# Optimization experiments

Hardware: AMD Instinct MI355X
Metric: run time of the kernel (lower is better)

The kernel has to match this reference:

```python
import jax, jax.numpy as jnp
import numpy as np

V, E, D, T, B = 32000, 512, 512, 512, 32
PAD = 3

def layer_norm(x, g, b, eps=1e-5):
    m = jnp.mean(x, axis=-1, keepdims=True)
    v = jnp.mean((x - m) ** 2, axis=-1, keepdims=True)
    return (x - m) * jax.lax.rsqrt(v + eps) * g + b

def sru_direction(U, v, b, reverse):
    # U: (T, B, 4D) -> splits: x_tilde, f-gate pre-act, r-gate pre-act, highway input
    x_t, uf, ur, xp = jnp.split(U, 4, axis=-1)
    def step(c, inp):
        xt, uft, urt, xpt = inp
        f = jax.nn.sigmoid(uft + v[0] * c + b[0])
        r = jax.nn.sigmoid(urt + v[1] * c + b[1])
        c_new = f * c + (1.0 - f) * xt
        h = r * c_new + (1.0 - r) * xpt
        return c_new, h
    c0 = jnp.zeros((U.shape[1], v.shape[1]), U.dtype)  # (B, D)
    c_last, hs = jax.lax.scan(step, c0, (x_t, uf, ur, xp), reverse=reverse)
    return hs, c_last

def setup_inputs() -> dict:
    key = jax.random.key(0)
    ks = jax.random.split(key, 8)
    def rn(k, shp, sc=0.05):
        return jax.random.normal(k, shp, jnp.float32) * sc
    return {
        "src": jax.random.randint(ks[0], (T, B), 0, V),
        "emb": rn(ks[1], (V, E), 0.1),
        "ln_g": jnp.ones((E,), jnp.float32),
        "ln_b": jnp.zeros((E,), jnp.float32),
        "W0": rn(ks[2], (E, 4 * D)),
        "W1": rn(ks[3], (E, 4 * D)),
        "v0": rn(ks[4], (2, D), 0.5),
        "v1": rn(ks[5], (2, D), 0.5),
        "b0": jnp.zeros((2, D), jnp.float32),
        "b1": jnp.zeros((2, D), jnp.float32),
        "W_out": rn(ks[6], (D, 2 * D)),
        "b_out": jnp.zeros((D,), jnp.float32),
    }

def reference(src, emb, ln_g, ln_b, W0, W1, v0, v1, b0, b1, W_out, b_out):
    table = emb.at[PAD].set(0.0)          # padding_idx row is zero
    x = table[src]                         # (T, B, E); dropout p=0 -> identity
    xn = layer_norm(x, ln_g, ln_b)         # SRU layer_norm=True: LN on cell input
    h0, c0 = sru_direction(jnp.einsum('tbe,ef->tbf', xn, W0), v0, b0, False)
    h1, c1 = sru_direction(jnp.einsum('tbe,ef->tbf', xn, W1), v1, b1, True)
    outputs = jnp.concatenate([h0, h1], axis=-1)        # (T, B, 2D)
    hidden = jnp.concatenate([c0, c1], axis=-1)[None]   # (1, B, 2D)
    out = jnp.tanh(jnp.einsum('tbh,dh->tbd', outputs, W_out) + b_out)
    return out, hidden
```

## Files before the change

### kernel.cpp

```cpp
#include <hip/hip_runtime.h>
#include <cstdint>
#include <cstddef>

#define T_DIM 512
#define B_DIM 32
#define E_DIM 512
#define D_DIM 512
#define PAD_IDX 3
#define M_ROWS (T_DIM * B_DIM)
#define PF 32

typedef __attribute__((ext_vector_type(8))) __bf16 bf16x8;
typedef __attribute__((ext_vector_type(4))) float  f32x4;

__device__ __forceinline__ unsigned short f2bf(float x) {
    union { float f; uint32_t u; } v; v.f = x;
    uint32_t u = v.u;
    uint32_t r = (u + 0x7FFFu + ((u >> 16) & 1u)) >> 16;
    return (unsigned short)r;
}
__device__ __forceinline__ float bf2f(unsigned short h) {
    union { float f; uint32_t u; } v; v.u = ((uint32_t)h) << 16;
    return v.f;
}
__device__ __forceinline__ float fast_sigmoid(float z) {
    return __builtin_amdgcn_rcpf(1.f + __expf(-z));
}
__device__ __forceinline__ float fast_tanh(float x) {
    return 1.f - 2.f * __builtin_amdgcn_rcpf(__expf(2.f * x) + 1.f);
}

__global__ __launch_bounds__(256) void wconv_kernel(
    const float* __restrict__ W0, const float* __restrict__ W1,
    unsigned short* __restrict__ Wt)
{
    __shared__ float tile[64][65];
    int k0  = blockIdx.x * 64;
    int n0g = blockIdx.y * 64;
    int dir = n0g >> 11;
    const float* W = dir ? W1 : W0;
    int d0 = (n0g & 2047) >> 2;
    int tx = threadIdx.x & 63;
    int ty = threadIdx.x >> 6;
    int scol = ((tx >> 4) << 9) + d0 + (tx & 15);
    for (int r = ty; r < 64; r += 4)
        tile[r][tx] = W[(size_t)(k0 + r) * 2048 + scol];
    __syncthreads();
    for (int r2 = ty; r2 < 64; r2 += 4) {
        int j = ((r2 & 3) << 4) | (r2 >> 2);
        Wt[(size_t)(n0g + r2) * 512 + k0 + tx] = f2bf(tile[tx][j]);
    }
}

__global__ __launch_bounds__(256) void bias_build_kernel(
    const float* __restrict__ b0, const float* __restrict__ b1,
    float* __restrict__ bias)
{
    int n = blockIdx.x * 256 + threadIdx.x;
    int dir = n >> 11, g = n & 3, d = (n & 2047) >> 2;
    const float* bp = dir ? b1 : b0;
    float v = (g == 1) ? bp[d] : ((g == 2) ? bp[512 + d] : 0.f);
    bias[n] = v;
}

__global__ __launch_bounds__(256) void woutconv_kernel(
    const float* __restrict__ W, unsigned short* __restrict__ O)
{
    int i = (blockIdx.x * 256 + threadIdx.x) * 4;
    f32x4 v = *(const f32x4*)(W + i);
    uint2 pk;
    pk.x = (uint32_t)f2bf(v[0]) | ((uint32_t)f2bf(v[1]) << 16);
    pk.y = (uint32_t)f2bf(v[2]) | ((uint32_t)f2bf(v[3]) << 16);
    *(uint2*)(O + i) = pk;
}

__global__ __launch_bounds__(256) void embed_ln_kernel(
    const int* __restrict__ src, const float* __restrict__ emb,
    const float* __restrict__ g, const float* __restrict__ bb,
    unsigned short* __restrict__ xn)
{
    int wave = threadIdx.x >> 6;
    int lane = threadIdx.x & 63;
    int row  = blockIdx.x * 4 + wave;
    int tok  = src[row];
    float x[8];
    if (tok == PAD_IDX) {
        #pragma unroll
        for (int j = 0; j < 8; j++) x[j] = 0.f;
    } else {
        const float* er = emb + (size_t)tok * E_DIM + lane * 8;
        f32x4 a0 = *(const f32x4*)(er);
        f32x4 a1 = *(const f32x4*)(er + 4);
        #pragma unroll
        for (int j = 0; j < 4; j++) { x[j] = a0[j]; x[4 + j] = a1[j]; }
    }
    float s = 0.f, sq = 0.f;
    #pragma unroll
    for (int j = 0; j < 8; j++) { s += x[j]; sq += x[j] * x[j]; }
    #pragma unroll
    for (int off = 32; off >= 1; off >>= 1) {
        s  += __shfl_xor(s,  off, 64);
        sq += __shfl_xor(sq, off, 64);
    }
    float mean = s * (1.f / 512.f);
    float var  = sq * (1.f / 512.f) - mean * mean;
    float rs   = rsqrtf(var + 1e-5f);
    f32x4 g0 = *(const f32x4*)(g + lane * 8);
    f32x4 g1 = *(const f32x4*)(g + lane * 8 + 4);
    f32x4 b0 = *(const f32x4*)(bb + lane * 8);
    f32x4 b1 = *(const f32x4*)(bb + lane * 8 + 4);
    unsigned short o[8];
    #pragma unroll
    for (int j = 0; j < 4; j++) {
        o[j]     = f2bf((x[j]     - mean) * rs * g0[j] + b0[j]);
        o[4 + j] = f2bf((x[4 + j] - mean) * rs * g1[j] + b1[j]);
    }
    uint4 pk;
    pk.x = (uint32_t)o[0] | ((uint32_t)o[1] << 16);
    pk.y = (uint32_t)o[2] | ((uint32_t)o[3] << 16);
    pk.z = (uint32_t)o[4] | ((uint32_t)o[5] << 16);
    pk.w = (uint32_t)o[6] | ((uint32_t)o[7] << 16);
    *(uint4*)(xn + (size_t)row * E_DIM + lane * 8) = pk;
}

template<int BM, int BN, int WM, int WN, int KD, int LOGNT, int EPI>
__global__ __launch_bounds__(512, 2) void gemm_pipe_kernel(
    const unsigned short* __restrict__ A,
    const unsigned short* __restrict__ Bt,
    void* __restrict__ Cout,
    const float* __restrict__ bias,
    int ldc)
{
    constexpr int NKT = KD / 32;
    constexpr int MR  = BM / WM / 16;
    constexpr int NR  = BN / WN / 16;
    constexpr int RA  = BM / 128;
    constexpr int RB  = BN / 128;
    constexpr int LPT = RA + RB;
    constexpr int ASZ = BM * 32;
    constexpr int BSZ = BN * 32;
    __shared__ unsigned short smem[4 * (ASZ + BSZ)];

    const int tid = threadIdx.x;
    const int w   = tid >> 6;
    const int l   = tid & 63;

    const int bid = blockIdx.x;
    const int cpx = gridDim.x >> 3;
    const int swz = (bid & 7) * cpx + (bid >> 3);
    const int mt  = swz >> LOGNT;
    const int nt  = swz & ((1 << LOGNT) - 1);

    const int wm = w / WN, wn = w % WN;

    const unsigned short* Ab = A  + (size_t)mt * BM * KD;
    const unsigned short* Bb = Bt + (size_t)nt * BN * KD;

    const int srow = w * 16 + (l >> 2);
    const int scol = ((l & 3) ^ ((l >> 3) & 3)) * 8;

    auto stage = [&](int t) {
        const unsigned short* Ag = Ab + t * 32;
        const unsigned short* Bg = Bb + t * 32;
        unsigned short* As = smem + (t & 3) * (ASZ + BSZ);
        unsigned short* Bs = As + ASZ;
        #pragma unroll
        for (int r = 0; r < RA; r++)
            __builtin_amdgcn_global_load_lds(
                (const __attribute__((address_space(1))) void*)(Ag + (size_t)(r * 128 + srow) * KD + scol),
                (__attribute__((address_space(3))) void*)(As + (r * 128 + w * 16) * 32),
                16, 0, 0);
        #pragma unroll
        for (int r = 0; r < RB; r++)
            __builtin_amdgcn_global_load_lds(
                (const __attribute__((address_space(1))) void*)(Bg + (size_t)(r * 128 + srow) * KD + scol),
                (__attribute__((address_space(3))) void*)(Bs + (r * 128 + w * 16) * 32),
                16, 0, 0);
    };

    f32x4 acc[MR][NR];
    #pragma unroll
    for (int m = 0; m < MR; m++)
        #pragma unroll
        for (int n = 0; n < NR; n++)
            acc[m][n] = (f32x4){0.f, 0.f, 0.f, 0.f};

    stage(0); stage(1); stage(2);

    const int li   = l & 15;
    const int cg   = l >> 4;
    const int rswz = (cg ^ ((li >> 1) & 3)) * 8;

    for (int t = 0; t < NKT; t++) {
        __builtin_amdgcn_sched_barrier(0);
        if (t + 2 < NKT)      asm volatile("s_waitcnt vmcnt(%0)" :: "n"(2 * LPT) : "memory");
        else if (t + 1 < NKT) asm volatile("s_waitcnt vmcnt(%0)" :: "n"(LPT) : "memory");
        else                  asm volatile("s_waitcnt vmcnt(0)" ::: "memory");
        __builtin_amdgcn_s_barrier();
        __builtin_amdgcn_sched_barrier(0);
        if (t + 3 < NKT) stage(t + 3);

        const unsigned short* As = smem + (t & 3) * (ASZ + BSZ);
        const unsigned short* Bs = As + ASZ;
        bf16x8 af[MR], bfv[NR];
        #pragma unroll
        for (int m = 0; m < MR; m++) {
            int row = wm * (BM / WM) + m * 16 + li;
            af[m] = *(const bf16x8*)(As + row * 32 + rswz);
        }
        #pragma unroll
        for (int n = 0; n < NR; n++) {
            int row = wn * (BN / WN) + n * 16 + li;
            bfv[n] = *(const bf16x8*)(Bs + row * 32 + rswz);
        }
        __builtin_amdgcn_s_setprio(1);
        #pragma unroll
        for (int m = 0; m < MR; m++)
            #pragma unroll
            for (int n = 0; n < NR; n++)
                acc[m][n] = __builtin_amdgcn_mfma_f32_16x16x32_bf16(
                    af[m], bfv[n], acc[m][n], 0, 0, 0);
        __builtin_amdgcn_s_setprio(0);
    }

    const int colb = nt * BN + wn * (BN / WN);
    const int rowb = mt * BM + wm * (BM / WM);
    #pragma unroll
    for (int m = 0; m < MR; m++) {
        #pragma unroll
        for (int n = 0; n < NR; n++) {
            int col  = colb + n * 16 + li;
            int row0 = rowb + m * 16 + cg * 4;
            float bi = bias[col];
            if (EPI == 0) {
                unsigned short* C = (unsigned short*)Cout;
                #pragma unroll
                for (int j = 0; j < 4; j++)
                    C[(size_t)(row0 + j) * ldc + col] = f2bf(acc[m][n][j] + bi);
            } else {
                float* C = (float*)Cout;
                #pragma unroll
                for (int j = 0; j < 4; j++)
                    C[(size_t)(row0 + j) * ldc + col] = fast_tanh(acc[m][n][j] + bi);
            }
        }
    }
}

__global__ __launch_bounds__(64) void sru_scan_kernel(
    const unsigned short* __restrict__ U,
    const float* __restrict__ v0, const float* __restrict__ v1,
    unsigned short* __restrict__ h,
    float* __restrict__ hidden)
{
    int id  = blockIdx.x * 64 + threadIdx.x;
    int dir = id >> 14;
    int rem = id & 16383;
    int b   = rem >> 9;
    int d   = rem & 511;
    const float* v = dir ? v1 : v0;
    float vf = v[d], vr = v[D_DIM + d];

    int row0  = (dir ? (T_DIM - 1) * B_DIM : 0) + b;
    long step = (long)(dir ? -B_DIM : B_DIM) * 1024;

    const ushort4* lp = (const ushort4*)U + (size_t)row0 * 1024 + dir * 512 + d;
    unsigned short* hp = h + (size_t)row0 * 1024 + dir * 512 + d;

    ushort4 buf[PF];
    #pragma unroll
    for (int p = 0; p < PF; p++) { buf[p] = *lp; lp += step; }

    float c = 0.f;
    for (int tb = 0; tb < T_DIM - PF; tb += PF) {
        #pragma unroll
        for (int p = 0; p < PF; p++) {
            ushort4 q = buf[p];
            buf[p] = *lp; lp += step;
            float x  = bf2f(q.x);
            float uf = bf2f(q.y);
            float ur = bf2f(q.z);
            float xp = bf2f(q.w);
            float f = fast_sigmoid(__fmaf_rn(vf, c, uf));
            float r = fast_sigmoid(__fmaf_rn(vr, c, ur));
            c = __fmaf_rn(f, c - x, x);
            float hv = __fmaf_rn(r, c - xp, xp);
            *hp = f2bf(hv); hp += step;
        }
    }
    #pragma unroll
    for (int p = 0; p < PF; p++) {
        ushort4 q = buf[p];
        float x  = bf2f(q.x);
        float uf = bf2f(q.y);
        float ur = bf2f(q.z);
        float xp = bf2f(q.w);
        float f = fast_sigmoid(__fmaf_rn(vf, c, uf));
        float r = fast_sigmoid(__fmaf_rn(vr, c, ur));
        c = __fmaf_rn(f, c - x, x);
        float hv = __fmaf_rn(r, c - xp, xp);
        *hp = f2bf(hv); hp += step;
    }
    hidden[b * 1024 + dir * 512 + d] = c;
}

extern "C" void kernel_launch(void* const* d_in, const int* in_sizes, int n_in,
                              void* d_out, int out_size, void* d_ws, size_t ws_size,
                              hipStream_t stream)
{
    const int*   src   = (const int*)  d_in[0];
    const float* emb   = (const float*)d_in[1];
    const float* ln_g  = (const float*)d_in[2];
    const float* ln_b  = (const float*)d_in[3];
    const float* W0    = (const float*)d_in[4];
    const float* W1    = (const float*)d_in[5];
    const float* v0    = (const float*)d_in[6];
    const float* v1    = (const float*)d_in[7];
    const float* b0    = (const float*)d_in[8];
    const float* b1    = (const float*)d_in[9];
    const float* W_out = (const float*)d_in[10];
    const float* b_out = (const float*)d_in[11];

    unsigned short* Wt  = (unsigned short*)d_ws;
    unsigned short* Wob = Wt  + (size_t)4096 * 512;
    unsigned short* xn  = Wob + (size_t)512 * 1024;
    unsigned short* U   = xn  + (size_t)M_ROWS * 512;
    unsigned short* h   = U   + (size_t)M_ROWS * 4096;
    float*          bias4096 = (float*)(h + (size_t)M_ROWS * 1024);

    float* out    = (float*)d_out;
    float* hidden = out + (size_t)M_ROWS * D_DIM;
    (void)out;

    wconv_kernel<<<dim3(8, 64), 256, 0, stream>>>(W0, W1, Wt);
    bias_build_kernel<<<16, 256, 0, stream>>>(b0, b1, bias4096);
    woutconv_kernel<<<512, 256, 0, stream>>>(W_out, Wob);
    embed_ln_kernel<<<M_ROWS / 4, 256, 0, stream>>>(src, emb, ln_g, ln_b, xn);

    gemm_pipe_kernel<256, 256, 2, 4, 512, 4, 0>
        <<<1024, 512, 0, stream>>>(xn, Wt, (void*)U, bias4096, 4096);

    sru_scan_kernel<<<512, 64, 0, stream>>>(U, v0, v1, h, hidden);

    gemm_pipe_kernel<256, 128, 4, 2, 1024, 2, 1>
        <<<256, 512, 0, stream>>>(h, Wob, (void*)d_out, b_out, 512);
}
```

Baseline: 174.2 us.

## Split GEMM k-step into two half-phases interleaving A/B staging with MFMA

Each k-iteration of the pipelined bf16 GEMM is split into two halves. The first half loads the B fragments and half of the A fragments and runs their MFMAs while only the next A tile is prefetched. After a second block barrier, the next B tile is prefetched and the other half of A is consumed. This spreads global-to-LDS traffic and LDS reads across the MFMA stream to hide latency better, at the cost of an extra barrier per k-step and fewer A fragments held in registers. The warp grid is also fixed at 2x4, which changes the output GEMM's warp tiling from 4x2.

```diff
diff --git a/kernel.cpp b/kernel.cpp
--- a/kernel.cpp
+++ b/kernel.cpp
@@ -123,7 +123,7 @@
     *(uint4*)(xn + (size_t)row * E_DIM + lane * 8) = pk;
 }
 
-template<int BM, int BN, int WM, int WN, int KD, int LOGNT, int EPI>
+template<int BM, int BN, int KD, int LOGNT, int EPI>
 __global__ __launch_bounds__(512, 2) void gemm_pipe_kernel(
     const unsigned short* __restrict__ A,
     const unsigned short* __restrict__ Bt,
@@ -131,9 +131,13 @@
     const float* __restrict__ bias,
     int ldc)
 {
+    constexpr int WM  = 2, WN = 4;
+    constexpr int WTM = BM / WM;
+    constexpr int WTN = BN / WN;
+    constexpr int MR  = WTM / 16;
+    constexpr int NR  = WTN / 16;
+    constexpr int MH  = MR / 2;
     constexpr int NKT = KD / 32;
-    constexpr int MR  = BM / WM / 16;
-    constexpr int NR  = BN / WN / 16;
     constexpr int RA  = BM / 128;
     constexpr int RB  = BN / 128;
     constexpr int LPT = RA + RB;
@@ -159,17 +163,19 @@
     const int srow = w * 16 + (l >> 2);
     const int scol = ((l & 3) ^ ((l >> 3) & 3)) * 8;
 
-    auto stage = [&](int t) {
+    auto stageA = [&](int t) {
         const unsigned short* Ag = Ab + t * 32;
-        const unsigned short* Bg = Bb + t * 32;
         unsigned short* As = smem + (t & 3) * (ASZ + BSZ);
-        unsigned short* Bs = As + ASZ;
         #pragma unroll
         for (int r = 0; r < RA; r++)
             __builtin_amdgcn_global_load_lds(
                 (const __attribute__((address_space(1))) void*)(Ag + (size_t)(r * 128 + srow) * KD + scol),
                 (__attribute__((address_space(3))) void*)(As + (r * 128 + w * 16) * 32),
                 16, 0, 0);
+    };
+    auto stageB = [&](int t) {
+        const unsigned short* Bg = Bb + t * 32;
+        unsigned short* Bs = smem + (t & 3) * (ASZ + BSZ) + ASZ;
         #pragma unroll
         for (int r = 0; r < RB; r++)
             __builtin_amdgcn_global_load_lds(
@@ -185,7 +191,7 @@
         for (int n = 0; n < NR; n++)
             acc[m][n] = (f32x4){0.f, 0.f, 0.f, 0.f};
 
-    stage(0); stage(1); stage(2);
+    stageA(0); stageB(0); stageA(1); stageB(1); stageA(2); stageB(2);
 
     const int li   = l & 15;
     const int cg   = l >> 4;
@@ -198,33 +204,56 @@
         else                  asm volatile("s_waitcnt vmcnt(0)" ::: "memory");
         __builtin_amdgcn_s_barrier();
         __builtin_amdgcn_sched_barrier(0);
-        if (t + 3 < NKT) stage(t + 3);
+        if (t + 3 < NKT) stageA(t + 3);
 
         const unsigned short* As = smem + (t & 3) * (ASZ + BSZ);
         const unsigned short* Bs = As + ASZ;
-        bf16x8 af[MR], bfv[NR];
-        #pragma unroll
-        for (int m = 0; m < MR; m++) {
-            int row = wm * (BM / WM) + m * 16 + li;
+        bf16x8 bfv[NR], af[MH];
+        #pragma unroll
+        for (int n = 0; n < NR; n++) {
+            int row = wn * WTN + n * 16 + li;
+            bfv[n] = *(const bf16x8*)(Bs + row * 32 + rswz);
+        }
+        #pragma unroll
+        for (int m = 0; m < MH; m++) {
+            int row = wm * WTM + m * 16 + li;
             af[m] = *(const bf16x8*)(As + row * 32 + rswz);
         }
-        #pragma unroll
-        for (int n = 0; n < NR; n++) {
-            int row = wn * (BN / WN) + n * 16 + li;
-            bfv[n] = *(const bf16x8*)(Bs + row * 32 + rswz);
-        }
+        asm volatile("s_waitcnt lgkmcnt(0)" ::: "memory");
+        __builtin_amdgcn_sched_barrier(0);
         __builtin_amdgcn_s_setprio(1);
         #pragma unroll
-        for (int m = 0; m < MR; m++)
+        for (int m = 0; m < MH; m++)
             #pragma unroll
             for (int n = 0; n < NR; n++)
                 acc[m][n] = __builtin_amdgcn_mfma_f32_16x16x32_bf16(
                     af[m], bfv[n], acc[m][n], 0, 0, 0);
         __builtin_amdgcn_s_setprio(0);
-    }
-
-    const int colb = nt * BN + wn * (BN / WN);
-    const int rowb = mt * BM + wm * (BM / WM);
+        __builtin_amdgcn_sched_barrier(0);
+        __builtin_amdgcn_s_barrier();
+        __builtin_amdgcn_sched_barrier(0);
+
+        if (t + 3 < NKT) stageB(t + 3);
+        #pragma unroll
+        for (int m = 0; m < MH; m++) {
+            int row = wm * WTM + (MH + m) * 16 + li;
+            af[m] = *(const bf16x8*)(As + row * 32 + rswz);
+        }
+        asm volatile("s_waitcnt lgkmcnt(0)" ::: "memory");
+        __builtin_amdgcn_sched_barrier(0);
+        __builtin_amdgcn_s_setprio(1);
+        #pragma unroll
+        for (int m = 0; m < MH; m++)
+            #pragma unroll
+            for (int n = 0; n < NR; n++)
+                acc[MH + m][n] = __builtin_amdgcn_mfma_f32_16x16x32_bf16(
+                    af[m], bfv[n], acc[MH + m][n], 0, 0, 0);
+        __builtin_amdgcn_s_setprio(0);
+        __builtin_amdgcn_sched_barrier(0);
+    }
+
+    const int colb = nt * BN + wn * WTN;
+    const int rowb = mt * BM + wm * WTM;
     #pragma unroll
     for (int m = 0; m < MR; m++) {
         #pragma unroll
@@ -337,11 +366,11 @@
     woutconv_kernel<<<512, 256, 0, stream>>>(W_out, Wob);
     embed_ln_kernel<<<M_ROWS / 4, 256, 0, stream>>>(src, emb, ln_g, ln_b, xn);
 
-    gemm_pipe_kernel<256, 256, 2, 4, 512, 4, 0>
+    gemm_pipe_kernel<256, 256, 512, 4, 0>
         <<<1024, 512, 0, stream>>>(xn, Wt, (void*)U, bias4096, 4096);
 
     sru_scan_kernel<<<512, 64, 0, stream>>>(U, v0, v1, h, hidden);
 
-    gemm_pipe_kernel<256, 128, 4, 2, 1024, 2, 1>
+    gemm_pipe_kernel<256, 128, 1024, 2, 1>
         <<<256, 512, 0, stream>>>(h, Wob, (void*)d_out, b_out, 512);
 }
```

Measured after the change: 176.3 us. About the same (+1.2%).

## Use 128x256 GEMM tiles with 3-stage LDS ring and grouped tile swizzle

Applied to the files above, without the earlier changes.

Both GEMMs now use a fixed 128x256 block tile with a 2x4 wave grid and 4x4 MFMA fragments per wave. The LDS ring drops from four stages to three, and launch bounds rise to four blocks per CU. Block-to-tile mapping moves to a grouped raster across the 8 XCDs to improve L2 reuse. The intent is higher occupancy and better cache locality, traded against a shallower prefetch depth and more blocks for the first GEMM.

```diff
diff --git a/kernel.cpp b/kernel.cpp
--- a/kernel.cpp
+++ b/kernel.cpp
@@ -123,35 +123,40 @@
     *(uint4*)(xn + (size_t)row * E_DIM + lane * 8) = pk;
 }
 
-template<int BM, int BN, int WM, int WN, int KD, int LOGNT, int EPI>
-__global__ __launch_bounds__(512, 2) void gemm_pipe_kernel(
+template<int KD, int NMT, int NNT, int GM, int GN, int EPI>
+__global__ __launch_bounds__(512, 4) void gemm_pipe_kernel(
     const unsigned short* __restrict__ A,
     const unsigned short* __restrict__ Bt,
     void* __restrict__ Cout,
     const float* __restrict__ bias,
     int ldc)
 {
+    constexpr int BM = 128, BN = 256;
+    constexpr int MR = 4, NR = 4;
     constexpr int NKT = KD / 32;
-    constexpr int MR  = BM / WM / 16;
-    constexpr int NR  = BN / WN / 16;
     constexpr int RA  = BM / 128;
     constexpr int RB  = BN / 128;
     constexpr int LPT = RA + RB;
     constexpr int ASZ = BM * 32;
     constexpr int BSZ = BN * 32;
-    __shared__ unsigned short smem[4 * (ASZ + BSZ)];
+    __shared__ unsigned short smem[3 * (ASZ + BSZ)];
 
     const int tid = threadIdx.x;
     const int w   = tid >> 6;
     const int l   = tid & 63;
 
+    constexpr int PER_G = GM * GN;
+    constexpr int NGC   = NNT / GN;
     const int bid = blockIdx.x;
-    const int cpx = gridDim.x >> 3;
-    const int swz = (bid & 7) * cpx + (bid >> 3);
-    const int mt  = swz >> LOGNT;
-    const int nt  = swz & ((1 << LOGNT) - 1);
-
-    const int wm = w / WN, wn = w % WN;
+    const int c   = bid & 7;
+    const int idx = bid >> 3;
+    const int gi  = idx / PER_G;
+    const int wi  = idx % PER_G;
+    const int gg  = c + 8 * gi;
+    const int mt  = (gg / NGC) * GM + wi / GN;
+    const int nt  = (gg % NGC) * GN + wi % GN;
+
+    const int wm = w >> 2, wn = w & 3;
 
     const unsigned short* Ab = A  + (size_t)mt * BM * KD;
     const unsigned short* Bb = Bt + (size_t)nt * BN * KD;
@@ -159,10 +164,10 @@
     const int srow = w * 16 + (l >> 2);
     const int scol = ((l & 3) ^ ((l >> 3) & 3)) * 8;
 
-    auto stage = [&](int t) {
+    auto stage = [&](int t, int slot) {
         const unsigned short* Ag = Ab + t * 32;
         const unsigned short* Bg = Bb + t * 32;
-        unsigned short* As = smem + (t & 3) * (ASZ + BSZ);
+        unsigned short* As = smem + slot * (ASZ + BSZ);
         unsigned short* Bs = As + ASZ;
         #pragma unroll
         for (int r = 0; r < RA; r++)
@@ -185,32 +190,32 @@
         for (int n = 0; n < NR; n++)
             acc[m][n] = (f32x4){0.f, 0.f, 0.f, 0.f};
 
-    stage(0); stage(1); stage(2);
+    stage(0, 0); stage(1, 1);
 
     const int li   = l & 15;
     const int cg   = l >> 4;
     const int rswz = (cg ^ ((li >> 1) & 3)) * 8;
 
+    int rs = 0, ss = 2;
     for (int t = 0; t < NKT; t++) {
-        __builtin_amdgcn_sched_barrier(0);
-        if (t + 2 < NKT)      asm volatile("s_waitcnt vmcnt(%0)" :: "n"(2 * LPT) : "memory");
-        else if (t + 1 < NKT) asm volatile("s_waitcnt vmcnt(%0)" :: "n"(LPT) : "memory");
-        else                  asm volatile("s_waitcnt vmcnt(0)" ::: "memory");
+        if (t + 1 < NKT)
+            asm volatile("s_waitcnt vmcnt(%0) lgkmcnt(0)" :: "n"(LPT) : "memory");
+        else
+            asm volatile("s_waitcnt vmcnt(0) lgkmcnt(0)" ::: "memory");
         __builtin_amdgcn_s_barrier();
-        __builtin_amdgcn_sched_barrier(0);
-        if (t + 3 < NKT) stage(t + 3);
-
-        const unsigned short* As = smem + (t & 3) * (ASZ + BSZ);
+        if (t + 2 < NKT) stage(t + 2, ss);
+
+        const unsigned short* As = smem + rs * (ASZ + BSZ);
         const unsigned short* Bs = As + ASZ;
         bf16x8 af[MR], bfv[NR];
         #pragma unroll
         for (int m = 0; m < MR; m++) {
-            int row = wm * (BM / WM) + m * 16 + li;
+            int row = wm * 64 + m * 16 + li;
             af[m] = *(const bf16x8*)(As + row * 32 + rswz);
         }
         #pragma unroll
         for (int n = 0; n < NR; n++) {
-            int row = wn * (BN / WN) + n * 16 + li;
+            int row = wn * 64 + n * 16 + li;
             bfv[n] = *(const bf16x8*)(Bs + row * 32 + rswz);
         }
         __builtin_amdgcn_s_setprio(1);
@@ -221,10 +226,13 @@
                 acc[m][n] = __builtin_amdgcn_mfma_f32_16x16x32_bf16(
                     af[m], bfv[n], acc[m][n], 0, 0, 0);
         __builtin_amdgcn_s_setprio(0);
-    }
-
-    const int colb = nt * BN + wn * (BN / WN);
-    const int rowb = mt * BM + wm * (BM / WM);
+
+        rs = (rs == 2) ? 0 : rs + 1;
+        ss = (ss == 2) ? 0 : ss + 1;
+    }
+
+    const int colb = nt * BN + wn * 64;
+    const int rowb = mt * BM + wm * 64;
     #pragma unroll
     for (int m = 0; m < MR; m++) {
         #pragma unroll
@@ -337,11 +345,11 @@
     woutconv_kernel<<<512, 256, 0, stream>>>(W_out, Wob);
     embed_ln_kernel<<<M_ROWS / 4, 256, 0, stream>>>(src, emb, ln_g, ln_b, xn);
 
-    gemm_pipe_kernel<256, 256, 2, 4, 512, 4, 0>
-        <<<1024, 512, 0, stream>>>(xn, Wt, (void*)U, bias4096, 4096);
+    gemm_pipe_kernel<512, 128, 16, 8, 4, 0>
+        <<<2048, 512, 0, stream>>>(xn, Wt, (void*)U, bias4096, 4096);
 
     sru_scan_kernel<<<512, 64, 0, stream>>>(U, v0, v1, h, hidden);
 
-    gemm_pipe_kernel<256, 128, 4, 2, 1024, 2, 1>
+    gemm_pipe_kernel<1024, 128, 2, 8, 2, 1>
         <<<256, 512, 0, stream>>>(h, Wob, (void*)d_out, b_out, 512);
 }
```

New measurement: 163.2 us. -6.3%, faster.
